# Performance work log

Measured on AMD Instinct MI355X. Metric: run time of the kernel, lower is better.

The kernel has to match this reference:

```python
import jax, jax.numpy as jnp
import numpy as np

B, S, E, H, V, C = 64, 512, 512, 1024, 32000, 20

def setup_inputs() -> dict:
    key = jax.random.key(0)
    ks = jax.random.split(key, 12)
    s_in = 1.0 / np.sqrt(E + H)
    s_h = 1.0 / np.sqrt(H)
    return {
        "x": jax.random.randint(ks[0], (B, S), 0, V),
        "label": jax.random.randint(ks[1], (B,), 0, C),
        "emb": jax.random.normal(ks[2], (V, E), dtype=jnp.float32),
        "Wf": jax.random.uniform(ks[3], (H, E + H), jnp.float32, -s_in, s_in),
        "bf": jnp.zeros((H,), jnp.float32),
        "Wi": jax.random.uniform(ks[4], (H, E + H), jnp.float32, -s_in, s_in),
        "bi": jnp.zeros((H,), jnp.float32),
        "Wc": jax.random.uniform(ks[5], (H, E + H), jnp.float32, -s_in, s_in),
        "bc": jnp.zeros((H,), jnp.float32),
        "Wo": jax.random.uniform(ks[6], (H, E + H), jnp.float32, -s_in, s_in),
        "bo": jnp.zeros((H,), jnp.float32),
        "Wv": jax.random.uniform(ks[7], (C, H), jnp.float32, -s_h, s_h),
        "bv": jnp.zeros((C,), jnp.float32),
    }

def _lstm_final(x_emb, Wf, bf, Wi, bi, Wc, bc, Wo, bo):
    # x_emb: [B, S, E]; returns final hidden state a [B, H]
    b = x_emb.shape[0]
    a0 = jnp.zeros((b, Wf.shape[0]), x_emb.dtype)
    c0 = jnp.zeros_like(a0)

    def step(carry, x_t):
        a_pre, c_pre = carry
        x_a = jnp.concatenate([x_t, a_pre], axis=1)  # [B, E+H]
        ft = jax.nn.sigmoid(x_a @ Wf.T + bf)
        it = jax.nn.sigmoid(x_a @ Wi.T + bi)
        cct = jnp.tanh(x_a @ Wc.T + bc)
        ot = jax.nn.sigmoid(x_a @ Wo.T + bo)
        c_next = ft * c_pre + it * cct
        a_next = jnp.tanh(c_next) * ot
        return (a_next, c_next), None

    (a_fin, _), _ = jax.lax.scan(step, (a0, c0), jnp.swapaxes(x_emb, 0, 1))
    return a_fin

def reference(x, label, emb, Wf, bf, Wi, bi, Wc, bc, Wo, bo, Wv, bv):
    x_emb = emb[x]                                   # [B, S, E]
    a_fin = _lstm_final(x_emb, Wf, bf, Wi, bi, Wc, bc, Wo, bo)
    logits = a_fin @ Wv.T + bv                       # [B, C]
    logp = jax.nn.log_softmax(logits, axis=-1)
    loss = -jnp.mean(logp[jnp.arange(logits.shape[0]), label])
    return loss
```

## Files before the change

### kernel.cpp

```cpp
#include <hip/hip_runtime.h>
#include <cstdint>
#include <cstddef>

typedef __bf16 bf16;
typedef __bf16 bf16x8 __attribute__((ext_vector_type(8)));
typedef __bf16 bf16x4 __attribute__((ext_vector_type(4)));
typedef float f32x4 __attribute__((ext_vector_type(4)));
typedef unsigned u32x4 __attribute__((ext_vector_type(4)));

#define B_ 64
#define S_ 512
#define E_ 512
#define H_ 1024
#define C_ 20
#define EH 1536
#define G4 4096

static const size_t OFF_WCAT  = 0;
static const size_t OFF_BIAS4 = 12582912;
static const size_t OFF_A0    = 12599296;
static const size_t OFF_A1    = 12730368;
static const size_t OFF_CST   = 12861440;
static const size_t OFF_LOSS  = 13123584;
static const size_t OFF_BAR   = 13123840;
static const size_t OFF_GX    = 13124864;
static const size_t STATE_BYTES = OFF_GX - OFF_A0;

__device__ inline float sigmoidf_(float x) { return 1.0f / (1.0f + __expf(-x)); }
__device__ inline float tanh_fast(float x) {
  float ax = fabsf(x);
  float e = __expf(-2.0f * ax);
  float t = (1.0f - e) / (1.0f + e);
  return copysignf(t, x);
}

__device__ inline void load_coh16(u32x4* dst, const void* p) {
  asm volatile("global_load_dwordx4 %0, %1, off sc0 sc1"
               : "=v"(*dst) : "v"(p) : "memory");
}

__global__ __launch_bounds__(256) void init_misc(uint4* st) {
  const int n = (int)(STATE_BYTES / 16);
  for (int idx = blockIdx.x * 256 + threadIdx.x; idx < n; idx += gridDim.x * 256)
    st[idx] = uint4{0u, 0u, 0u, 0u};
}

__global__ __launch_bounds__(256) void convert_w(
    const float* __restrict__ Wf, const float* __restrict__ Wi,
    const float* __restrict__ Wc, const float* __restrict__ Wo,
    const float* __restrict__ bfp, const float* __restrict__ bip,
    const float* __restrict__ bcp, const float* __restrict__ bop,
    bf16* __restrict__ Wcat, float* __restrict__ bias4)
{
  const int total = G4 * (EH / 8);
  for (int idx = blockIdx.x * 256 + threadIdx.x; idx < total; idx += gridDim.x * 256) {
    const int r = idx / 192;
    const int ck = idx - r * 192;
    const int g = r & 3, h = r >> 2;
    const float* W = (g == 0) ? Wf : (g == 1) ? Wi : (g == 2) ? Wc : Wo;
    const float* src = W + (size_t)h * EH + ck * 8;
    const float4 v0 = *(const float4*)src;
    const float4 v1 = *(const float4*)(src + 4);
    bf16x8 o;
    o[0] = (bf16)v0.x; o[1] = (bf16)v0.y; o[2] = (bf16)v0.z; o[3] = (bf16)v0.w;
    o[4] = (bf16)v1.x; o[5] = (bf16)v1.y; o[6] = (bf16)v1.z; o[7] = (bf16)v1.w;
    *(bf16x8*)(Wcat + (size_t)r * EH + ck * 8) = o;
    if (ck == 0) {
      const float* Bp = (g == 0) ? bfp : (g == 1) ? bip : (g == 2) ? bcp : bop;
      bias4[r] = Bp[h];
    }
  }
}

__global__ __launch_bounds__(256) void gemm_gx(
    const int* __restrict__ x, const float* __restrict__ emb,
    const bf16* __restrict__ Wcat, bf16* __restrict__ gx, int t0)
{
  __shared__ char As[16384];
  __shared__ char Bs[16384];
  const int t = threadIdx.x;
  const int lane = t & 63, wid = t >> 6;
  const int wm = wid >> 1, wn = wid & 1;
  const int bm = blockIdx.x >> 5;
  const int bn = blockIdx.x & 31;
  const int m0l = bm * 128, n0 = bn * 128;
  f32x4 acc[4][4] = {};
  const int srow = t >> 3, sc16 = t & 7;
  for (int k0 = 0; k0 < E_; k0 += 64) {
    __syncthreads();
    #pragma unroll
    for (int i = 0; i < 4; ++i) {
      const int row = i * 32 + srow;
      const int cs = sc16 ^ (row & 7);
      const int m = t0 * 64 + m0l + row;
      const int tok = x[(m & 63) * S_ + (m >> 6)];
      const float* srcA = emb + (size_t)tok * E_ + k0 + cs * 8;
      const float4 a0v = *(const float4*)srcA;
      const float4 a1v = *(const float4*)(srcA + 4);
      bf16x8 oa;
      oa[0] = (bf16)a0v.x; oa[1] = (bf16)a0v.y; oa[2] = (bf16)a0v.z; oa[3] = (bf16)a0v.w;
      oa[4] = (bf16)a1v.x; oa[5] = (bf16)a1v.y; oa[6] = (bf16)a1v.z; oa[7] = (bf16)a1v.w;
      *(bf16x8*)(As + row * 128 + sc16 * 16) = oa;
      const uint4 vb = *(const uint4*)(Wcat + (size_t)(n0 + row) * EH + k0 + cs * 8);
      *(uint4*)(Bs + row * 128 + sc16 * 16) = vb;
    }
    __syncthreads();
    #pragma unroll
    for (int ks = 0; ks < 64; ks += 32) {
      const int kb = (ks + ((lane >> 4) * 8)) * 2;
      bf16x8 af[4], bfr[4];
      #pragma unroll
      for (int mt = 0; mt < 4; ++mt) {
        const int ra = wm * 64 + mt * 16 + (lane & 15);
        af[mt] = *(const bf16x8*)(As + ra * 128 + (kb ^ ((ra & 7) << 4)));
      }
      #pragma unroll
      for (int nt = 0; nt < 4; ++nt) {
        const int rb = wn * 64 + nt * 16 + (lane & 15);
        bfr[nt] = *(const bf16x8*)(Bs + rb * 128 + (kb ^ ((rb & 7) << 4)));
      }
      #pragma unroll
      for (int mt = 0; mt < 4; ++mt)
        #pragma unroll
        for (int nt = 0; nt < 4; ++nt)
          acc[mt][nt] = __builtin_amdgcn_mfma_f32_16x16x32_bf16(af[mt], bfr[nt], acc[mt][nt], 0, 0, 0);
    }
  }
  const int cb = (lane >> 4) * 4;
  #pragma unroll
  for (int mt = 0; mt < 4; ++mt) {
    #pragma unroll
    for (int r = 0; r < 4; ++r) {
      const int mrow = m0l + wm * 64 + mt * 16 + cb + r;
      bf16* dst = gx + (size_t)mrow * G4 + n0 + wn * 64 + (lane & 15);
      #pragma unroll
      for (int nt = 0; nt < 4; ++nt)
        dst[nt * 16] = (bf16)acc[mt][nt][r];
    }
  }
}

__global__ __launch_bounds__(256, 1) void lstm_rec(
    const bf16* __restrict__ Wcat, const float* __restrict__ bias4,
    const bf16* __restrict__ gx, bf16* __restrict__ a0,
    bf16* __restrict__ a1, float* __restrict__ cstg,
    unsigned* __restrict__ bar, int t0, int tc)
{
  __shared__ float accs[4][16][68];
  const int t = threadIdx.x;
  const int lane = t & 63;
  const int w = t >> 6;
  const int bid = blockIdx.x;
  const int grp = bid & 3;
  const int hwg = bid >> 2;
  const int h0 = hwg * 16;
  const int l15 = lane & 15;
  const int kq = (lane >> 4) * 8;

  bf16x8 wf[32];
  {
    const bf16* wbase = Wcat + (size_t)(h0 * 4 + l15) * EH + 512 + w * 256 + kq;
    #pragma unroll
    for (int nt = 0; nt < 4; ++nt)
      #pragma unroll
      for (int i = 0; i < 8; ++i)
        wf[nt * 8 + i] = *(const bf16x8*)(wbase + (size_t)nt * 16 * EH + i * 32);
  }
  const int j   = t & 15;
  const int blb = t >> 4;
  const float4 bias = *(const float4*)(bias4 + (h0 + j) * 4);
  const int bg0 = grp * 16 + blb;
  float cst = cstg[(size_t)bg0 * H_ + h0 + j];
  unsigned* flags = bar + grp * 64;
  unsigned* myflag = flags + w * 16 + l15;

  for (int s = 0; s < tc; ++s) {
    const int step = t0 + s;
    const bf16* aprev = (step & 1) ? a1 : a0;
    bf16* anext = (step & 1) ? a0 : a1;
    const bf16* gxrow = gx + (size_t)s * (B_ * G4);
    const bf16x4 g0 = *(const bf16x4*)(gxrow + (size_t)bg0 * G4 + (h0 + j) * 4);
    {
      unsigned v;
      do {
        v = __hip_atomic_load(myflag, __ATOMIC_RELAXED, __HIP_MEMORY_SCOPE_AGENT);
      } while (v < (unsigned)step);
    }
    __builtin_amdgcn_sched_barrier(0);
    const bf16* abase = aprev + (size_t)(grp * 16 + l15) * H_ + w * 256 + kq;
    u32x4 af[8];
    #pragma unroll
    for (int i = 0; i < 8; ++i) load_coh16(&af[i], abase + i * 32);
    asm volatile("s_waitcnt vmcnt(0)" ::: "memory");
    __builtin_amdgcn_sched_barrier(0);
    f32x4 pacc[4] = {};
    #pragma unroll
    for (int i = 0; i < 8; ++i) {
      const bf16x8 a8 = __builtin_bit_cast(bf16x8, af[i]);
      #pragma unroll
      for (int nt = 0; nt < 4; ++nt)
        pacc[nt] = __builtin_amdgcn_mfma_f32_16x16x32_bf16(a8, wf[nt * 8 + i], pacc[nt], 0, 0, 0);
    }
    __syncthreads();
    {
      const int m0 = (lane >> 4) * 4;
      #pragma unroll
      for (int nt = 0; nt < 4; ++nt)
        #pragma unroll
        for (int r = 0; r < 4; ++r)
          accs[w][m0 + r][nt * 16 + l15] = pacc[nt][r];
    }
    __syncthreads();
    const float4 q0 = *(const float4*)&accs[0][blb][j * 4];
    const float4 q1 = *(const float4*)&accs[1][blb][j * 4];
    const float4 q2 = *(const float4*)&accs[2][blb][j * 4];
    const float4 q3 = *(const float4*)&accs[3][blb][j * 4];
    float hv;
    {
      const float pf = q0.x + q1.x + q2.x + q3.x + (float)g0[0] + bias.x;
      const float pi = q0.y + q1.y + q2.y + q3.y + (float)g0[1] + bias.y;
      const float pc = q0.z + q1.z + q2.z + q3.z + (float)g0[2] + bias.z;
      const float po = q0.w + q1.w + q2.w + q3.w + (float)g0[3] + bias.w;
      const float fg = sigmoidf_(pf), ig = sigmoidf_(pi), og = sigmoidf_(po);
      cst = fg * cst + ig * tanh_fast(pc);
      hv = tanh_fast(cst) * og;
    }
    {
      const unsigned u0 = (unsigned)__builtin_bit_cast(unsigned short, (bf16)hv);
      const unsigned n0 = __shfl_down(u0, 1);
      if ((j & 1) == 0) {
        unsigned* an = (unsigned*)anext;
        __hip_atomic_store(an + ((size_t)bg0 * H_ + h0 + j) / 2, u0 | (n0 << 16),
                           __ATOMIC_RELAXED, __HIP_MEMORY_SCOPE_AGENT);
      }
    }
    __syncthreads();
    if (t == 0) {
      __hip_atomic_store(flags + hwg, (unsigned)(step + 1),
                         __ATOMIC_RELAXED, __HIP_MEMORY_SCOPE_AGENT);
    }
  }
  cstg[(size_t)bg0 * H_ + h0 + j] = cst;
}

__global__ __launch_bounds__(256) void logits_loss(
    const bf16* __restrict__ afin, const float* __restrict__ Wv,
    const float* __restrict__ bv, const int* __restrict__ label,
    float* __restrict__ lossa)
{
  const int b = blockIdx.x;
  const int t = threadIdx.x;
  const int lane = t & 63, wid = t >> 6;
  const bf16x4 a4 = *(const bf16x4*)(afin + (size_t)b * H_ + t * 4);
  const float av0 = (float)a4[0], av1 = (float)a4[1], av2 = (float)a4[2], av3 = (float)a4[3];
  float part[C_];
  #pragma unroll
  for (int c = 0; c < C_; ++c) {
    const float4 w = *(const float4*)(Wv + (size_t)c * H_ + t * 4);
    part[c] = av0 * w.x + av1 * w.y + av2 * w.z + av3 * w.w;
  }
  #pragma unroll
  for (int off = 32; off > 0; off >>= 1) {
    #pragma unroll
    for (int c = 0; c < C_; ++c) part[c] += __shfl_down(part[c], off);
  }
  __shared__ float red[4][C_];
  __shared__ float lg[C_];
  if (lane == 0) {
    #pragma unroll
    for (int c = 0; c < C_; ++c) red[wid][c] = part[c];
  }
  __syncthreads();
  if (t < C_) lg[t] = red[0][t] + red[1][t] + red[2][t] + red[3][t] + bv[t];
  __syncthreads();
  if (t == 0) {
    float m = lg[0];
    for (int c = 1; c < C_; ++c) m = fmaxf(m, lg[c]);
    float se = 0.0f;
    for (int c = 0; c < C_; ++c) se += __expf(lg[c] - m);
    const float lse = logf(se) + m;
    lossa[b] = lse - lg[label[b]];
  }
}

__global__ __launch_bounds__(64) void loss_mean(const float* __restrict__ lossa,
                                                float* __restrict__ out) {
  const int t = threadIdx.x;
  float v = lossa[t];
  #pragma unroll
  for (int off = 32; off > 0; off >>= 1) v += __shfl_down(v, off);
  if (t == 0) out[0] = v * (1.0f / 64.0f);
}

extern "C" void kernel_launch(void* const* d_in, const int* in_sizes, int n_in,
                              void* d_out, int out_size, void* d_ws, size_t ws_size,
                              hipStream_t stream) {
  const int*   x     = (const int*)d_in[0];
  const int*   label = (const int*)d_in[1];
  const float* emb   = (const float*)d_in[2];
  const float* Wf    = (const float*)d_in[3];
  const float* bfp   = (const float*)d_in[4];
  const float* Wi    = (const float*)d_in[5];
  const float* bip   = (const float*)d_in[6];
  const float* Wc    = (const float*)d_in[7];
  const float* bcp   = (const float*)d_in[8];
  const float* Wo    = (const float*)d_in[9];
  const float* bop   = (const float*)d_in[10];
  const float* Wv    = (const float*)d_in[11];
  const float* bv    = (const float*)d_in[12];
  (void)in_sizes; (void)n_in; (void)out_size;

  int TC = 0;
  const size_t avail = (ws_size > OFF_GX) ? (ws_size - OFF_GX) : 0;
  const int cands[7] = {512, 256, 128, 64, 32, 16, 8};
  for (int i = 0; i < 7; ++i) {
    if ((size_t)cands[i] * 524288 <= avail) { TC = cands[i]; break; }
  }
  if (TC == 0) return;

  char* ws = (char*)d_ws;
  bf16*     Wcat  = (bf16*)(ws + OFF_WCAT);
  float*    bias4 = (float*)(ws + OFF_BIAS4);
  bf16*     a0    = (bf16*)(ws + OFF_A0);
  bf16*     a1    = (bf16*)(ws + OFF_A1);
  float*    cstg  = (float*)(ws + OFF_CST);
  float*    lossa = (float*)(ws + OFF_LOSS);
  unsigned* bar   = (unsigned*)(ws + OFF_BAR);
  bf16*     gx    = (bf16*)(ws + OFF_GX);

  init_misc<<<64, 256, 0, stream>>>((uint4*)(ws + OFF_A0));
  convert_w<<<1024, 256, 0, stream>>>(Wf, Wi, Wc, Wo, bfp, bip, bcp, bop, Wcat, bias4);
  const int nchunks = S_ / TC;
  for (int c = 0; c < nchunks; ++c) {
    const int t0 = c * TC;
    gemm_gx<<<(TC / 2) * 32, 256, 0, stream>>>(x, emb, Wcat, gx, t0);
    lstm_rec<<<256, 256, 0, stream>>>(Wcat, bias4, gx, a0, a1, cstg, bar, t0, TC);
  }
  logits_loss<<<64, 256, 0, stream>>>(a0, Wv, bv, label, lossa);
  loss_mean<<<1, 64, 0, stream>>>(lossa, (float*)d_out);
}
```

Baseline: 2.122 ms.

## Replace flag barrier with step-tagged hidden-state packets in LSTM recurrence

The hidden state is now stored as 16-byte packets, each holding four bf16 values plus the step number as a tag. Readers spin directly on the data loads until every tag matches, so the separate per-block flag store and the extra __syncthreads that guarded it are gone. The LDS reduction buffer is double-buffered by step parity, which removes one more barrier per step. In exchange, the hidden-state buffers double in size and every poll reloads the full operand set.

```diff
diff --git a/kernel.cpp b/kernel.cpp
--- a/kernel.cpp
+++ b/kernel.cpp
@@ -18,13 +18,12 @@
 
 static const size_t OFF_WCAT  = 0;
 static const size_t OFF_BIAS4 = 12582912;
-static const size_t OFF_A0    = 12599296;
-static const size_t OFF_A1    = 12730368;
-static const size_t OFF_CST   = 12861440;
-static const size_t OFF_LOSS  = 13123584;
-static const size_t OFF_BAR   = 13123840;
-static const size_t OFF_GX    = 13124864;
-static const size_t STATE_BYTES = OFF_GX - OFF_A0;
+static const size_t OFF_AT0   = 12599296;
+static const size_t OFF_AT1   = 12861440;
+static const size_t OFF_CST   = 13123584;
+static const size_t OFF_LOSS  = 13385728;
+static const size_t OFF_GX    = 13385984;
+static const size_t STATE_BYTES = OFF_GX - OFF_AT0;
 
 __device__ inline float sigmoidf_(float x) { return 1.0f / (1.0f + __expf(-x)); }
 __device__ inline float tanh_fast(float x) {
@@ -33,10 +32,18 @@
   float t = (1.0f - e) / (1.0f + e);
   return copysignf(t, x);
 }
+__device__ inline float bf2f(unsigned lo16) {
+  const unsigned u = lo16 << 16;
+  return __builtin_bit_cast(float, u);
+}
 
 __device__ inline void load_coh16(u32x4* dst, const void* p) {
   asm volatile("global_load_dwordx4 %0, %1, off sc0 sc1"
                : "=v"(*dst) : "v"(p) : "memory");
+}
+__device__ inline void store_coh16(void* p, u32x4 v) {
+  asm volatile("global_store_dwordx4 %0, %1, off sc0 sc1"
+               :: "v"(p), "v"(v) : "memory");
 }
 
 __global__ __launch_bounds__(256) void init_misc(uint4* st) {
@@ -142,11 +149,11 @@
 
 __global__ __launch_bounds__(256, 1) void lstm_rec(
     const bf16* __restrict__ Wcat, const float* __restrict__ bias4,
-    const bf16* __restrict__ gx, bf16* __restrict__ a0,
-    bf16* __restrict__ a1, float* __restrict__ cstg,
-    unsigned* __restrict__ bar, int t0, int tc)
+    const bf16* __restrict__ gx, unsigned* __restrict__ at0,
+    unsigned* __restrict__ at1, float* __restrict__ cstg,
+    int t0, int tc)
 {
-  __shared__ float accs[4][16][68];
+  __shared__ __align__(16) float accs[2][4][16][68];
   const int t = threadIdx.x;
   const int lane = t & 63;
   const int w = t >> 6;
@@ -155,11 +162,11 @@
   const int hwg = bid >> 2;
   const int h0 = hwg * 16;
   const int l15 = lane & 15;
-  const int kq = (lane >> 4) * 8;
+  const int kq8 = (lane >> 4) * 8;
 
   bf16x8 wf[32];
   {
-    const bf16* wbase = Wcat + (size_t)(h0 * 4 + l15) * EH + 512 + w * 256 + kq;
+    const bf16* wbase = Wcat + (size_t)(h0 * 4 + l15) * EH + 512 + w * 256 + kq8;
     #pragma unroll
     for (int nt = 0; nt < 4; ++nt)
       #pragma unroll
@@ -171,50 +178,58 @@
   const float4 bias = *(const float4*)(bias4 + (h0 + j) * 4);
   const int bg0 = grp * 16 + blb;
   float cst = cstg[(size_t)bg0 * H_ + h0 + j];
-  unsigned* flags = bar + grp * 64;
-  unsigned* myflag = flags + w * 16 + l15;
+  const size_t aboff = ((size_t)(grp * 16 + l15) * 256 + (size_t)(w * 64 + (lane >> 4) * 2)) * 4;
+  const size_t pgoff = ((size_t)bg0 * 256 + (size_t)((h0 >> 2) + (j >> 2))) * 4;
 
   for (int s = 0; s < tc; ++s) {
     const int step = t0 + s;
-    const bf16* aprev = (step & 1) ? a1 : a0;
-    bf16* anext = (step & 1) ? a0 : a1;
-    const bf16* gxrow = gx + (size_t)s * (B_ * G4);
-    const bf16x4 g0 = *(const bf16x4*)(gxrow + (size_t)bg0 * G4 + (h0 + j) * 4);
-    {
-      unsigned v;
-      do {
-        v = __hip_atomic_load(myflag, __ATOMIC_RELAXED, __HIP_MEMORY_SCOPE_AGENT);
-      } while (v < (unsigned)step);
+    const unsigned exp_tag = (unsigned)step;
+    const unsigned* aprev = (step & 1) ? at1 : at0;
+    unsigned* anext = (step & 1) ? at0 : at1;
+    const bf16x4 g0 = *(const bf16x4*)(gx + (size_t)s * (B_ * G4) + (size_t)bg0 * G4 + (h0 + j) * 4);
+
+    const unsigned* abase = aprev + aboff;
+    u32x4 g[16];
+    for (;;) {
+      #pragma unroll
+      for (int i = 0; i < 8; ++i) {
+        load_coh16(&g[2 * i],     abase + i * 32);
+        load_coh16(&g[2 * i + 1], abase + i * 32 + 4);
+      }
+      asm volatile("s_waitcnt vmcnt(0)" ::: "memory");
+      __builtin_amdgcn_sched_barrier(0);
+      int ok = 1;
+      #pragma unroll
+      for (int i = 0; i < 16; ++i) ok &= (g[i].z == exp_tag) ? 1 : 0;
+      if (__all(ok)) break;
     }
     __builtin_amdgcn_sched_barrier(0);
-    const bf16* abase = aprev + (size_t)(grp * 16 + l15) * H_ + w * 256 + kq;
-    u32x4 af[8];
-    #pragma unroll
-    for (int i = 0; i < 8; ++i) load_coh16(&af[i], abase + i * 32);
-    asm volatile("s_waitcnt vmcnt(0)" ::: "memory");
-    __builtin_amdgcn_sched_barrier(0);
+
     f32x4 pacc[4] = {};
     #pragma unroll
     for (int i = 0; i < 8; ++i) {
-      const bf16x8 a8 = __builtin_bit_cast(bf16x8, af[i]);
+      u32x4 mg;
+      mg.x = g[2 * i].x; mg.y = g[2 * i].y;
+      mg.z = g[2 * i + 1].x; mg.w = g[2 * i + 1].y;
+      const bf16x8 a8 = __builtin_bit_cast(bf16x8, mg);
       #pragma unroll
       for (int nt = 0; nt < 4; ++nt)
         pacc[nt] = __builtin_amdgcn_mfma_f32_16x16x32_bf16(a8, wf[nt * 8 + i], pacc[nt], 0, 0, 0);
     }
-    __syncthreads();
+    const int par = step & 1;
     {
       const int m0 = (lane >> 4) * 4;
       #pragma unroll
       for (int nt = 0; nt < 4; ++nt)
         #pragma unroll
         for (int r = 0; r < 4; ++r)
-          accs[w][m0 + r][nt * 16 + l15] = pacc[nt][r];
+          accs[par][w][m0 + r][nt * 16 + l15] = pacc[nt][r];
     }
     __syncthreads();
-    const float4 q0 = *(const float4*)&accs[0][blb][j * 4];
-    const float4 q1 = *(const float4*)&accs[1][blb][j * 4];
-    const float4 q2 = *(const float4*)&accs[2][blb][j * 4];
-    const float4 q3 = *(const float4*)&accs[3][blb][j * 4];
+    const float4 q0 = *(const float4*)&accs[par][0][blb][j * 4];
+    const float4 q1 = *(const float4*)&accs[par][1][blb][j * 4];
+    const float4 q2 = *(const float4*)&accs[par][2][blb][j * 4];
+    const float4 q3 = *(const float4*)&accs[par][3][blb][j * 4];
     float hv;
     {
       const float pf = q0.x + q1.x + q2.x + q3.x + (float)g0[0] + bias.x;
@@ -226,33 +241,30 @@
       hv = tanh_fast(cst) * og;
     }
     {
-      const unsigned u0 = (unsigned)__builtin_bit_cast(unsigned short, (bf16)hv);
-      const unsigned n0 = __shfl_down(u0, 1);
-      if ((j & 1) == 0) {
-        unsigned* an = (unsigned*)anext;
-        __hip_atomic_store(an + ((size_t)bg0 * H_ + h0 + j) / 2, u0 | (n0 << 16),
-                           __ATOMIC_RELAXED, __HIP_MEMORY_SCOPE_AGENT);
+      const unsigned me = (unsigned)__builtin_bit_cast(unsigned short, (bf16)hv);
+      const unsigned pr  = me | (__shfl_down(me, 1) << 16);
+      const unsigned pr2 = __shfl_down(pr, 2);
+      if ((j & 3) == 0) {
+        u32x4 outq;
+        outq.x = pr; outq.y = pr2; outq.z = (unsigned)(step + 1); outq.w = 0u;
+        store_coh16(anext + pgoff, outq);
       }
     }
-    __syncthreads();
-    if (t == 0) {
-      __hip_atomic_store(flags + hwg, (unsigned)(step + 1),
-                         __ATOMIC_RELAXED, __HIP_MEMORY_SCOPE_AGENT);
-    }
   }
   cstg[(size_t)bg0 * H_ + h0 + j] = cst;
 }
 
 __global__ __launch_bounds__(256) void logits_loss(
-    const bf16* __restrict__ afin, const float* __restrict__ Wv,
+    const unsigned* __restrict__ at, const float* __restrict__ Wv,
     const float* __restrict__ bv, const int* __restrict__ label,
     float* __restrict__ lossa)
 {
   const int b = blockIdx.x;
   const int t = threadIdx.x;
   const int lane = t & 63, wid = t >> 6;
-  const bf16x4 a4 = *(const bf16x4*)(afin + (size_t)b * H_ + t * 4);
-  const float av0 = (float)a4[0], av1 = (float)a4[1], av2 = (float)a4[2], av3 = (float)a4[3];
+  const u32x4 gv = *(const u32x4*)(at + ((size_t)b * 256 + t) * 4);
+  const float av0 = bf2f(gv.x & 0xffffu), av1 = bf2f(gv.x >> 16);
+  const float av2 = bf2f(gv.y & 0xffffu), av3 = bf2f(gv.y >> 16);
   float part[C_];
   #pragma unroll
   for (int c = 0; c < C_; ++c) {
@@ -321,21 +333,20 @@
   char* ws = (char*)d_ws;
   bf16*     Wcat  = (bf16*)(ws + OFF_WCAT);
   float*    bias4 = (float*)(ws + OFF_BIAS4);
-  bf16*     a0    = (bf16*)(ws + OFF_A0);
-  bf16*     a1    = (bf16*)(ws + OFF_A1);
+  unsigned* at0   = (unsigned*)(ws + OFF_AT0);
+  unsigned* at1   = (unsigned*)(ws + OFF_AT1);
   float*    cstg  = (float*)(ws + OFF_CST);
   float*    lossa = (float*)(ws + OFF_LOSS);
-  unsigned* bar   = (unsigned*)(ws + OFF_BAR);
   bf16*     gx    = (bf16*)(ws + OFF_GX);
 
-  init_misc<<<64, 256, 0, stream>>>((uint4*)(ws + OFF_A0));
+  init_misc<<<64, 256, 0, stream>>>((uint4*)(ws + OFF_AT0));
   convert_w<<<1024, 256, 0, stream>>>(Wf, Wi, Wc, Wo, bfp, bip, bcp, bop, Wcat, bias4);
   const int nchunks = S_ / TC;
   for (int c = 0; c < nchunks; ++c) {
     const int t0 = c * TC;
     gemm_gx<<<(TC / 2) * 32, 256, 0, stream>>>(x, emb, Wcat, gx, t0);
-    lstm_rec<<<256, 256, 0, stream>>>(Wcat, bias4, gx, a0, a1, cstg, bar, t0, TC);
-  }
-  logits_loss<<<64, 256, 0, stream>>>(a0, Wv, bv, label, lossa);
+    lstm_rec<<<256, 256, 0, stream>>>(Wcat, bias4, gx, at0, at1, cstg, t0, TC);
+  }
+  logits_loss<<<64, 256, 0, stream>>>(at0, Wv, bv, label, lossa);
   loss_mean<<<1, 64, 0, stream>>>(lossa, (float*)d_out);
 }
```

Result: slower. 2.598 ms (+22.5%).

## Use per-wave fine-grained flags and double-buffered LDS in LSTM recurrence

Applied to the files above, without the earlier changes.

Replaces the one-flag-per-workgroup barrier with per-wave flags (4 per workgroup). Each lane polls flags for just the chunks of the previous hidden state it needs and issues each payload load as soon as its producer is ready. The LDS reduction buffer is double-buffered by step parity, which removes the trailing __syncthreads per step, and hidden-state writes are packed into dwordx2 stores. The aim is to shorten the cross-workgroup synchronization latency on the 512-step serial critical path, at the cost of more flag traffic and polling loads.

```diff
diff --git a/kernel.cpp b/kernel.cpp
--- a/kernel.cpp
+++ b/kernel.cpp
@@ -7,6 +7,7 @@
 typedef __bf16 bf16x4 __attribute__((ext_vector_type(4)));
 typedef float f32x4 __attribute__((ext_vector_type(4)));
 typedef unsigned u32x4 __attribute__((ext_vector_type(4)));
+typedef unsigned u32x2 __attribute__((ext_vector_type(2)));
 
 #define B_ 64
 #define S_ 512
@@ -23,7 +24,7 @@
 static const size_t OFF_CST   = 12861440;
 static const size_t OFF_LOSS  = 13123584;
 static const size_t OFF_BAR   = 13123840;
-static const size_t OFF_GX    = 13124864;
+static const size_t OFF_GX    = 13127936;
 static const size_t STATE_BYTES = OFF_GX - OFF_A0;
 
 __device__ inline float sigmoidf_(float x) { return 1.0f / (1.0f + __expf(-x)); }
@@ -32,11 +33,6 @@
   float e = __expf(-2.0f * ax);
   float t = (1.0f - e) / (1.0f + e);
   return copysignf(t, x);
-}
-
-__device__ inline void load_coh16(u32x4* dst, const void* p) {
-  asm volatile("global_load_dwordx4 %0, %1, off sc0 sc1"
-               : "=v"(*dst) : "v"(p) : "memory");
 }
 
 __global__ __launch_bounds__(256) void init_misc(uint4* st) {
@@ -146,7 +142,7 @@
     bf16* __restrict__ a1, float* __restrict__ cstg,
     unsigned* __restrict__ bar, int t0, int tc)
 {
-  __shared__ float accs[4][16][68];
+  __shared__ __align__(16) float accs[2][4][16][68];
   const int t = threadIdx.x;
   const int lane = t & 63;
   const int w = t >> 6;
@@ -155,11 +151,12 @@
   const int hwg = bid >> 2;
   const int h0 = hwg * 16;
   const int l15 = lane & 15;
-  const int kq = (lane >> 4) * 8;
+  const int ksub = lane >> 4;
+  const int kq8 = ksub * 8;
 
   bf16x8 wf[32];
   {
-    const bf16* wbase = Wcat + (size_t)(h0 * 4 + l15) * EH + 512 + w * 256 + kq;
+    const bf16* wbase = Wcat + (size_t)(h0 * 4 + l15) * EH + 512 + w * 256 + kq8;
     #pragma unroll
     for (int nt = 0; nt < 4; ++nt)
       #pragma unroll
@@ -171,50 +168,65 @@
   const float4 bias = *(const float4*)(bias4 + (h0 + j) * 4);
   const int bg0 = grp * 16 + blb;
   float cst = cstg[(size_t)bg0 * H_ + h0 + j];
-  unsigned* flags = bar + grp * 64;
-  unsigned* myflag = flags + w * 16 + l15;
+  unsigned* gflags = bar + grp * 256;
+  unsigned* fbase = gflags + (16 * w + (ksub >> 1)) * 4 + (l15 >> 2);
+  const size_t pbase = (size_t)(grp * 16 + l15) * H_ + w * 256 + kq8;
+  unsigned* myflag = gflags + hwg * 4 + w;
 
   for (int s = 0; s < tc; ++s) {
     const int step = t0 + s;
+    const unsigned tgt = (unsigned)step;
     const bf16* aprev = (step & 1) ? a1 : a0;
     bf16* anext = (step & 1) ? a0 : a1;
-    const bf16* gxrow = gx + (size_t)s * (B_ * G4);
-    const bf16x4 g0 = *(const bf16x4*)(gxrow + (size_t)bg0 * G4 + (h0 + j) * 4);
-    {
-      unsigned v;
-      do {
-        v = __hip_atomic_load(myflag, __ATOMIC_RELAXED, __HIP_MEMORY_SCOPE_AGENT);
-      } while (v < (unsigned)step);
-    }
-    __builtin_amdgcn_sched_barrier(0);
-    const bf16* abase = aprev + (size_t)(grp * 16 + l15) * H_ + w * 256 + kq;
-    u32x4 af[8];
-    #pragma unroll
-    for (int i = 0; i < 8; ++i) load_coh16(&af[i], abase + i * 32);
+    const bf16x4 g0 = *(const bf16x4*)(gx + (size_t)s * (B_ * G4) + (size_t)bg0 * G4 + (h0 + j) * 4);
+
+    u32x4 pay[8];
+    unsigned fv[8];
+    unsigned need = 0xffu;
+    while (need) {
+      #pragma unroll
+      for (int i = 0; i < 8; ++i) {
+        if (need & (1u << i)) {
+          asm volatile("global_load_dword %0, %1, off sc0 sc1"
+                       : "=v"(fv[i]) : "v"(fbase + 8 * i) : "memory");
+        }
+      }
+      asm volatile("s_waitcnt vmcnt(0)" ::: "memory");
+      __builtin_amdgcn_sched_barrier(0);
+      #pragma unroll
+      for (int i = 0; i < 8; ++i) {
+        if ((need & (1u << i)) && fv[i] >= tgt) {
+          asm volatile("global_load_dwordx4 %0, %1, off sc0 sc1"
+                       : "=v"(pay[i]) : "v"(aprev + pbase + i * 32) : "memory");
+          need &= ~(1u << i);
+        }
+      }
+    }
     asm volatile("s_waitcnt vmcnt(0)" ::: "memory");
     __builtin_amdgcn_sched_barrier(0);
+
     f32x4 pacc[4] = {};
     #pragma unroll
     for (int i = 0; i < 8; ++i) {
-      const bf16x8 a8 = __builtin_bit_cast(bf16x8, af[i]);
+      const bf16x8 a8 = __builtin_bit_cast(bf16x8, pay[i]);
       #pragma unroll
       for (int nt = 0; nt < 4; ++nt)
         pacc[nt] = __builtin_amdgcn_mfma_f32_16x16x32_bf16(a8, wf[nt * 8 + i], pacc[nt], 0, 0, 0);
     }
-    __syncthreads();
+    const int par = step & 1;
     {
-      const int m0 = (lane >> 4) * 4;
+      const int m0 = ksub * 4;
       #pragma unroll
       for (int nt = 0; nt < 4; ++nt)
         #pragma unroll
         for (int r = 0; r < 4; ++r)
-          accs[w][m0 + r][nt * 16 + l15] = pacc[nt][r];
+          accs[par][w][m0 + r][nt * 16 + l15] = pacc[nt][r];
     }
     __syncthreads();
-    const float4 q0 = *(const float4*)&accs[0][blb][j * 4];
-    const float4 q1 = *(const float4*)&accs[1][blb][j * 4];
-    const float4 q2 = *(const float4*)&accs[2][blb][j * 4];
-    const float4 q3 = *(const float4*)&accs[3][blb][j * 4];
+    const float4 q0 = *(const float4*)&accs[par][0][blb][j * 4];
+    const float4 q1 = *(const float4*)&accs[par][1][blb][j * 4];
+    const float4 q2 = *(const float4*)&accs[par][2][blb][j * 4];
+    const float4 q3 = *(const float4*)&accs[par][3][blb][j * 4];
     float hv;
     {
       const float pf = q0.x + q1.x + q2.x + q3.x + (float)g0[0] + bias.x;
@@ -226,18 +238,21 @@
       hv = tanh_fast(cst) * og;
     }
     {
-      const unsigned u0 = (unsigned)__builtin_bit_cast(unsigned short, (bf16)hv);
-      const unsigned n0 = __shfl_down(u0, 1);
-      if ((j & 1) == 0) {
-        unsigned* an = (unsigned*)anext;
-        __hip_atomic_store(an + ((size_t)bg0 * H_ + h0 + j) / 2, u0 | (n0 << 16),
-                           __ATOMIC_RELAXED, __HIP_MEMORY_SCOPE_AGENT);
-      }
-    }
-    __syncthreads();
-    if (t == 0) {
-      __hip_atomic_store(flags + hwg, (unsigned)(step + 1),
-                         __ATOMIC_RELAXED, __HIP_MEMORY_SCOPE_AGENT);
+      const unsigned me = (unsigned)__builtin_bit_cast(unsigned short, (bf16)hv);
+      const unsigned pr  = me | (__shfl_down(me, 1) << 16);
+      const unsigned pr2 = __shfl_down(pr, 2);
+      if ((j & 3) == 0) {
+        u32x2 pv; pv.x = pr; pv.y = pr2;
+        asm volatile("global_store_dwordx2 %0, %1, off sc0 sc1"
+                     :: "v"(anext + (size_t)bg0 * H_ + h0 + j), "v"(pv) : "memory");
+      }
+    }
+    asm volatile("s_waitcnt vmcnt(0)" ::: "memory");
+    __builtin_amdgcn_sched_barrier(0);
+    if (lane == 0) {
+      const unsigned nf = (unsigned)(step + 1);
+      asm volatile("global_store_dword %0, %1, off sc0 sc1"
+                   :: "v"(myflag), "v"(nf) : "memory");
     }
   }
   cstg[(size_t)bg0 * H_ + h0 + j] = cst;
```

Measured after the change: 3.086 ms. +45.4%, slower.
